# Kernel tuning notes

Hardware: AMD Instinct MI355X
Metric: run time of the kernel (lower is better)

## Reference

```python
import jax, jax.numpy as jnp
import numpy as np

N, C, T, V = 64, 64, 256, 25
REL, OUT = 8, 64
ALPHA = 1.0


def setup_inputs() -> dict:
    key = jax.random.key(0)
    ks = jax.random.split(key, 10)
    s = lambda k, shape: jax.random.normal(k, shape, dtype=jnp.float32) * 0.05
    return {
        "x": jax.random.normal(ks[0], (N, C, T, V), dtype=jnp.float32),
        "A": jax.random.normal(ks[1], (V, V), dtype=jnp.float32),
        "w1": s(ks[2], (REL, C)), "b1": s(ks[3], (REL,)),
        "w2": s(ks[4], (REL, C)), "b2": s(ks[5], (REL,)),
        "w3": s(ks[6], (OUT, C)), "b3": s(ks[7], (OUT,)),
        "w4": s(ks[8], (OUT, REL)), "b4": s(ks[9], (OUT,)),
    }


def reference(x, A, w1, b1, w2, b2, w3, b3, w4, b4):
    # 1x1 conv commutes with the temporal mean, so reduce T first (same math).
    xm = jnp.mean(x, axis=2)                                   # [N, C, V]
    x1 = jnp.einsum('ncv,rc->nrv', xm, w1) + b1[:, None]        # [N, R, V]
    x2 = jnp.einsum('ncv,rc->nrv', xm, w2) + b2[:, None]        # [N, R, V]
    x3 = jnp.einsum('nctv,oc->notv', x, w3) + b3[:, None, None] # [N, O, T, V]
    # dynamic topology: tanh of broadcast difference -> [N, R, V, V]
    adj = jnp.tanh(x1[:, :, :, None] - x2[:, :, None, :])
    # conv4 (1x1 over VxV) then scale + static adjacency
    d = jnp.einsum('nruv,or->nouv', adj, w4) + b4[:, None, None]
    d = d * ALPHA + A[None, None]                               # [N, O, V, V]
    # graph aggregation: out[n,o,t,v] = sum_u d[n,o,u,v] * x3[n,o,t,u]
    return jnp.einsum('nouv,notu->notv', d, x3)
```

## Files before the change

### kernel.cpp

```cpp
#include <hip/hip_runtime.h>

#define N_ 64
#define C_ 64
#define T_ 256
#define V_ 25
#define R_ 8
#define O_ 64
constexpr int TV = T_ * V_;
constexpr float INV_T = 1.0f / (float)T_;
constexpr int TC = 16;
constexpr int NPOS = TC * V_;
constexpr int NT = NPOS / 16;
constexpr int DP = 32;
constexpr int UPAD = 40;
constexpr int X3S = 16 * UPAD + 8;
constexpr int LS = 402;

typedef __attribute__((ext_vector_type(8))) short s8v;
typedef __attribute__((ext_vector_type(4))) float f4v;

__device__ __forceinline__ unsigned short f2bf(float f) {
    union { float f; unsigned u; } v; v.f = f;
    unsigned r = v.u + 0x7FFFu + ((v.u >> 16) & 1u);
    return (unsigned short)(r >> 16);
}
__device__ __forceinline__ unsigned pk2(float a, float b) {
    return (unsigned)f2bf(a) | ((unsigned)f2bf(b) << 16);
}
__device__ __forceinline__ float bf2f(unsigned short h) {
    union { unsigned u; float f; } v; v.u = (unsigned)h << 16; return v.f;
}

__global__ __launch_bounds__(512) void k_prep(const float* __restrict__ x,
                                              float* __restrict__ xm,
                                              float* out) {
    __shared__ unsigned short lx[C_ * LS];
    const int n   = blockIdx.y;
    const int tc  = blockIdx.x;
    const int tid = threadIdx.x;
    const float* xb = x + (size_t)n * C_ * TV + tc * NPOS;
    char* xTb = (char*)out + (size_t)n * O_ * TV * 4 + (size_t)tc * 1600;

    #pragma unroll 4
    for (int i = 0; i < 13; ++i) {
        const int s = i * 512 + tid;
        if (s < C_ * 100) {
            const int c = s / 100, p4 = s - c * 100;
            const f4v v = *(const f4v*)(xb + (size_t)c * TV + p4 * 4);
            unsigned* p = (unsigned*)&lx[c * LS + p4 * 4];
            p[0] = pk2(v[0], v[1]);
            p[1] = pk2(v[2], v[3]);
        }
    }
    __syncthreads();

    #pragma unroll
    for (int i = 0; i < 4; ++i) {
        const int p = i * 512 + tid;
        if (p < C_ * V_) {
            const int c = p / V_, v = p - c * V_;
            float s = 0.f;
            #pragma unroll
            for (int t = 0; t < TC; ++t) s += bf2f(lx[c * LS + t * V_ + v]);
            atomicAdd(&xm[(size_t)n * C_ * V_ + p], s * INV_T);
        }
    }

    #pragma unroll 2
    for (int i = 0; i < 7; ++i) {
        const int it = i * 512 + tid;
        if (it < 3200) {
            const int pos = it >> 3, ch = it & 7;
            s8v pk;
            #pragma unroll
            for (int j = 0; j < 8; ++j)
                pk[j] = (short)lx[(ch * 8 + j) * LS + pos];
            const int L = pos * 128 + ch * 16;
            const int row = L / 1600, off = L - row * 1600;
            *(s8v*)(xTb + (size_t)row * (TV * 4) + off) = pk;
        }
    }
}

__global__ __launch_bounds__(256) void k_dmat(const float* __restrict__ xm,
                                              const float* __restrict__ A,
                                              const float* __restrict__ w1,
                                              const float* __restrict__ b1,
                                              const float* __restrict__ w2,
                                              const float* __restrict__ b2,
                                              const float* __restrict__ w4,
                                              const float* __restrict__ b4,
                                              unsigned short* __restrict__ dT) {
    __shared__ float xms[C_][V_];
    __shared__ float x1s[R_][V_];
    __shared__ float x2s[R_][V_];
    const int n  = blockIdx.x;
    const int og = blockIdx.y * 8;
    const int tid = threadIdx.x;

    for (int i = tid; i < C_ * V_; i += 256)
        xms[i / V_][i % V_] = xm[(size_t)n * C_ * V_ + i];
    __syncthreads();

    for (int i = tid; i < 2 * R_ * V_; i += 256) {
        const int j = i % (R_ * V_);
        const int r = j / V_, v = j % V_;
        const bool first = (i < R_ * V_);
        const float* w = first ? w1 : w2;
        float acc = first ? b1[r] : b2[r];
        #pragma unroll
        for (int c = 0; c < C_; ++c) acc += w[r * C_ + c] * xms[c][v];
        if (first) x1s[r][v] = acc;
        else       x2s[r][v] = acc;
    }
    __syncthreads();

    unsigned short* dn = dT + (size_t)n * O_ * DP * DP;
    for (int p = tid; p < DP * DP; p += 256) {
        const int v = p >> 5, u = p & 31;
        if (u < V_ && v < V_) {
            float adjr[R_];
            #pragma unroll
            for (int r = 0; r < R_; ++r) adjr[r] = tanhf(x1s[r][u] - x2s[r][v]);
            const float a = A[u * V_ + v];
            #pragma unroll
            for (int oo = 0; oo < 8; ++oo) {
                const int o = og + oo;
                float acc = b4[o];
                #pragma unroll
                for (int r = 0; r < R_; ++r) acc = fmaf(w4[o * R_ + r], adjr[r], acc);
                dn[(size_t)o * DP * DP + p] = f2bf(acc + a);
            }
        } else {
            #pragma unroll
            for (int oo = 0; oo < 8; ++oo)
                dn[(size_t)(og + oo) * DP * DP + p] = 0;
        }
    }
}

__global__ __launch_bounds__(512) void k_F(const float* __restrict__ w3,
                                           const float* __restrict__ b3,
                                           const unsigned short* __restrict__ dT,
                                           float* io) {
    __shared__ __align__(16) unsigned short x3b[16 * X3S];

    const int n    = blockIdx.y;
    const int tc   = blockIdx.x;
    const int tid  = threadIdx.x;
    const int lane = tid & 63;
    const int wave = tid >> 6;
    const int l16  = lane & 15;
    const int lg   = lane >> 4;

    if (tid < 256) {
        const int o_l = tid >> 4, t = tid & 15;
        *(s8v*)&x3b[o_l * X3S + t * UPAD + 24] = (s8v)0;
    }
    __syncthreads();

    const char* xTb = (const char*)io + (size_t)n * O_ * TV * 4 + (size_t)tc * 1600;
    s8v bfr[4][2];
    #pragma unroll
    for (int i = 0; i < 4; ++i) {
        const int nt = wave + 8 * i;
        if (nt < NT) {
            const int pos = nt * 16 + l16;
            #pragma unroll
            for (int kh = 0; kh < 2; ++kh) {
                const int L = pos * 128 + kh * 64 + lg * 16;
                const int row = L / 1600, off = L - row * 1600;
                bfr[i][kh] = *(const s8v*)(xTb + (size_t)row * (TV * 4) + off);
            }
        }
    }

    const unsigned short* dn = dT + (size_t)n * O_ * DP * DP;
    float* on = io + (size_t)n * O_ * TV + tc * NPOS;

    #pragma unroll 1
    for (int h = 0; h < 4; ++h) {
        s8v afr[2];
        #pragma unroll
        for (int kh = 0; kh < 2; ++kh) {
            const float* wp = w3 + (h * 16 + l16) * C_ + kh * 32 + lg * 8;
            s8v f;
            #pragma unroll
            for (int j = 0; j < 8; ++j) f[j] = (short)f2bf(wp[j]);
            afr[kh] = f;
        }
        const f4v b3h = *(const f4v*)(b3 + h * 16 + lg * 4);

        #pragma unroll
        for (int i = 0; i < 4; ++i) {
            const int nt = wave + 8 * i;
            if (nt < NT) {
                const int pos = nt * 16 + l16;
                const int t = pos / 25, u = pos - 25 * t;
                f4v acc = (f4v)0.f;
                acc = __builtin_amdgcn_mfma_f32_16x16x32_bf16(afr[0], bfr[i][0], acc, 0, 0, 0);
                acc = __builtin_amdgcn_mfma_f32_16x16x32_bf16(afr[1], bfr[i][1], acc, 0, 0, 0);
                #pragma unroll
                for (int r = 0; r < 4; ++r)
                    x3b[(lg * 4 + r) * X3S + t * UPAD + u] = f2bf(acc[r] + b3h[r]);
            }
        }
        __syncthreads();

        #pragma unroll
        for (int oo = 0; oo < 2; ++oo) {
            const int o_l = wave * 2 + oo;
            const int o_g = h * 16 + o_l;
            const unsigned short* dp = dn + (size_t)o_g * DP * DP;
            const s8v bv0 = *(const s8v*)(dp + l16 * DP + lg * 8);
            const s8v bv1 = *(const s8v*)(dp + (16 + l16) * DP + lg * 8);
            const s8v av  = *(const s8v*)&x3b[o_l * X3S + l16 * UPAD + lg * 8];
            f4v c0 = (f4v)0.f, c1 = (f4v)0.f;
            c0 = __builtin_amdgcn_mfma_f32_16x16x32_bf16(av, bv0, c0, 0, 0, 0);
            c1 = __builtin_amdgcn_mfma_f32_16x16x32_bf16(av, bv1, c1, 0, 0, 0);
            float* ob = on + (size_t)o_g * TV;
            #pragma unroll
            for (int r = 0; r < 4; ++r) {
                const int t = lg * 4 + r;
                ob[t * 25 + l16] = c0[r];
                if (l16 < 9) ob[t * 25 + 16 + l16] = c1[r];
            }
        }
        __syncthreads();
    }
}

extern "C" void kernel_launch(void* const* d_in, const int* in_sizes, int n_in,
                              void* d_out, int out_size, void* d_ws, size_t ws_size,
                              hipStream_t stream) {
    const float* x  = (const float*)d_in[0];
    const float* A  = (const float*)d_in[1];
    const float* w1 = (const float*)d_in[2];
    const float* b1 = (const float*)d_in[3];
    const float* w2 = (const float*)d_in[4];
    const float* b2 = (const float*)d_in[5];
    const float* w3 = (const float*)d_in[6];
    const float* b3 = (const float*)d_in[7];
    const float* w4 = (const float*)d_in[8];
    const float* b4 = (const float*)d_in[9];

    float* out = (float*)d_out;
    float* xm  = (float*)d_ws;
    unsigned short* dTm = (unsigned short*)(xm + (size_t)N_ * C_ * V_);

    hipMemsetAsync(xm, 0, (size_t)N_ * C_ * V_ * sizeof(float), stream);
    k_prep<<<dim3(T_ / TC, N_), 512, 0, stream>>>(x, xm, out);
    k_dmat<<<dim3(N_, 8), 256, 0, stream>>>(xm, A, w1, b1, w2, b2, w4, b4, dTm);
    k_F<<<dim3(T_ / TC, N_), 512, 0, stream>>>(w3, b3, dTm, out);
}
```

Before: 97.45 us.

## Replace LDS transpose and temporal reduction in prep kernel with MFMA identity/selector matmuls

The prep kernel no longer stages x in shared memory. Each wave loads bf16-packed fragments straight into registers. It uses MFMA against an identity matrix to transpose channels into the packed output layout, and MFMA against a position-mod-25 selector matrix to accumulate the temporal sums per joint. This removes the LDS round trip, the __syncthreads barrier and the strided LDS reads. In exchange it adds redundant matrix-core work, narrower 8-byte global stores, and clamped overlapping loads on the last chunk.

```diff
diff --git a/kernel.cpp b/kernel.cpp
--- a/kernel.cpp
+++ b/kernel.cpp
@@ -14,10 +14,10 @@
 constexpr int DP = 32;
 constexpr int UPAD = 40;
 constexpr int X3S = 16 * UPAD + 8;
-constexpr int LS = 402;
 
 typedef __attribute__((ext_vector_type(8))) short s8v;
 typedef __attribute__((ext_vector_type(4))) float f4v;
+typedef __attribute__((ext_vector_type(2))) unsigned u2v;
 
 __device__ __forceinline__ unsigned short f2bf(float f) {
     union { float f; unsigned u; } v; v.f = f;
@@ -27,58 +27,92 @@
 __device__ __forceinline__ unsigned pk2(float a, float b) {
     return (unsigned)f2bf(a) | ((unsigned)f2bf(b) << 16);
 }
-__device__ __forceinline__ float bf2f(unsigned short h) {
-    union { unsigned u; float f; } v; v.u = (unsigned)h << 16; return v.f;
-}
 
 __global__ __launch_bounds__(512) void k_prep(const float* __restrict__ x,
                                               float* __restrict__ xm,
                                               float* out) {
-    __shared__ unsigned short lx[C_ * LS];
-    const int n   = blockIdx.y;
-    const int tc  = blockIdx.x;
-    const int tid = threadIdx.x;
-    const float* xb = x + (size_t)n * C_ * TV + tc * NPOS;
+    const int n    = blockIdx.y;
+    const int tc   = blockIdx.x;
+    const int tid  = threadIdx.x;
+    const int lane = tid & 63;
+    const int wave = tid >> 6;
+    const int cq   = wave & 3;
+    const int half = wave >> 2;
+    const int l16  = lane & 15;
+    const int lg   = lane >> 4;
+
+    const float* xr = x + (size_t)(n * C_ + cq * 16 + l16) * TV + tc * NPOS;
     char* xTb = (char*)out + (size_t)n * O_ * TV * 4 + (size_t)tc * 1600;
 
-    #pragma unroll 4
-    for (int i = 0; i < 13; ++i) {
-        const int s = i * 512 + tid;
-        if (s < C_ * 100) {
-            const int c = s / 100, p4 = s - c * 100;
-            const f4v v = *(const f4v*)(xb + (size_t)c * TV + p4 * 4);
-            unsigned* p = (unsigned*)&lx[c * LS + p4 * 4];
-            p[0] = pk2(v[0], v[1]);
-            p[1] = pk2(v[2], v[3]);
-        }
-    }
-    __syncthreads();
-
+    s8v bi_lo, bi_hi;
     #pragma unroll
-    for (int i = 0; i < 4; ++i) {
-        const int p = i * 512 + tid;
-        if (p < C_ * V_) {
-            const int c = p / V_, v = p - c * V_;
-            float s = 0.f;
-            #pragma unroll
-            for (int t = 0; t < TC; ++t) s += bf2f(lx[c * LS + t * V_ + v]);
-            atomicAdd(&xm[(size_t)n * C_ * V_ + p], s * INV_T);
-        }
-    }
-
-    #pragma unroll 2
-    for (int i = 0; i < 7; ++i) {
-        const int it = i * 512 + tid;
-        if (it < 3200) {
-            const int pos = it >> 3, ch = it & 7;
-            s8v pk;
-            #pragma unroll
-            for (int j = 0; j < 8; ++j)
-                pk[j] = (short)lx[(ch * 8 + j) * LS + pos];
-            const int L = pos * 128 + ch * 16;
-            const int row = L / 1600, off = L - row * 1600;
-            *(s8v*)(xTb + (size_t)row * (TV * 4) + off) = pk;
-        }
+    for (int j = 0; j < 8; ++j) {
+        const int k = lg * 8 + j;
+        bi_lo[j] = (short)((k == l16)      ? 0x3F80 : 0);
+        bi_hi[j] = (short)((k == l16 + 16) ? 0x3F80 : 0);
+    }
+
+    f4v acc0 = (f4v)0.f, acc1 = (f4v)0.f;
+
+    const int ch0 = half * 7, ch1 = half ? 13 : 7;
+    #pragma unroll 1
+    for (int ch = ch0; ch < ch1; ++ch) {
+        const int posbase = ch * 32;
+        int off = posbase + lg * 8;
+        if (off >= NPOS) off = NPOS - 16;
+        const f4v xa = *(const f4v*)(xr + off);
+        const f4v xb = *(const f4v*)(xr + off + 4);
+        s8v afr;
+        {
+            unsigned* ap = (unsigned*)&afr;
+            ap[0] = pk2(xa[0], xa[1]); ap[1] = pk2(xa[2], xa[3]);
+            ap[2] = pk2(xb[0], xb[1]); ap[3] = pk2(xb[2], xb[3]);
+        }
+
+        f4v c0 = (f4v)0.f, c1 = (f4v)0.f;
+        c0 = __builtin_amdgcn_mfma_f32_16x16x32_bf16(afr, bi_lo, c0, 0, 0, 0);
+        c1 = __builtin_amdgcn_mfma_f32_16x16x32_bf16(afr, bi_hi, c1, 0, 0, 0);
+
+        s8v bm_lo, bm_hi;
+        {
+            const int kb = posbase + lg * 8;
+            int m = kb % 25;
+            #pragma unroll
+            for (int j = 0; j < 8; ++j) {
+                const bool valid = (kb + j) < NPOS;
+                bm_lo[j] = (short)((valid && m == l16)      ? 0x3F80 : 0);
+                bm_hi[j] = (short)((valid && m == l16 + 16) ? 0x3F80 : 0);
+                if (++m == 25) m = 0;
+            }
+        }
+        acc0 = __builtin_amdgcn_mfma_f32_16x16x32_bf16(afr, bm_lo, acc0, 0, 0, 0);
+        acc1 = __builtin_amdgcn_mfma_f32_16x16x32_bf16(afr, bm_hi, acc1, 0, 0, 0);
+
+        {
+            const int pos = posbase + l16;
+            const int L = pos * 128 + (cq * 16 + lg * 4) * 2;
+            const int row = L / 1600, o = L - row * 1600;
+            *(u2v*)(xTb + (size_t)row * (TV * 4) + o) =
+                u2v{pk2(c0[0], c0[1]), pk2(c0[2], c0[3])};
+        }
+        if (posbase + 16 + l16 < NPOS) {
+            const int pos = posbase + 16 + l16;
+            const int L = pos * 128 + (cq * 16 + lg * 4) * 2;
+            const int row = L / 1600, o = L - row * 1600;
+            *(u2v*)(xTb + (size_t)row * (TV * 4) + o) =
+                u2v{pk2(c1[0], c1[1]), pk2(c1[2], c1[3])};
+        }
+    }
+
+    const int cb = cq * 16 + lg * 4;
+    float* xb0 = xm + (size_t)n * C_ * V_;
+    #pragma unroll
+    for (int r = 0; r < 4; ++r)
+        atomicAdd(&xb0[(cb + r) * V_ + l16], acc0[r] * INV_T);
+    if (l16 < 9) {
+        #pragma unroll
+        for (int r = 0; r < 4; ++r)
+            atomicAdd(&xb0[(cb + r) * V_ + 16 + l16], acc1[r] * INV_T);
     }
 }
 
```

Result: slower. 110.6 us (+13.5%).

## Split prep blocks in half and replace atomic mean with partial-sum reduction kernel

Applied to the files above, without the earlier changes.

Each prep block now handles half of a 16-timestep chunk (200 positions) with 256 threads, doubling the grid and halving shared memory per block. Instead of atomically accumulating the temporal mean into a zeroed buffer, each block writes its per-block partial sums to a workspace, and a new reduction kernel sums the 32 partials per sample. This removes the memset and the atomic contention, and may raise occupancy. The cost is an extra kernel launch and additional workspace traffic for the partial sums.

```diff
diff --git a/kernel.cpp b/kernel.cpp
--- a/kernel.cpp
+++ b/kernel.cpp
@@ -14,7 +14,8 @@
 constexpr int DP = 32;
 constexpr int UPAD = 40;
 constexpr int X3S = 16 * UPAD + 8;
-constexpr int LS = 402;
+constexpr int CV = C_ * V_;
+constexpr int LSTR = 210;
 
 typedef __attribute__((ext_vector_type(8))) short s8v;
 typedef __attribute__((ext_vector_type(4))) float f4v;
@@ -31,54 +32,73 @@
     union { unsigned u; float f; } v; v.u = (unsigned)h << 16; return v.f;
 }
 
-__global__ __launch_bounds__(512) void k_prep(const float* __restrict__ x,
-                                              float* __restrict__ xm,
+__global__ __launch_bounds__(256) void k_prep(const float* __restrict__ x,
+                                              float* __restrict__ xmp,
                                               float* out) {
-    __shared__ unsigned short lx[C_ * LS];
-    const int n   = blockIdx.y;
-    const int tc  = blockIdx.x;
-    const int tid = threadIdx.x;
-    const float* xb = x + (size_t)n * C_ * TV + tc * NPOS;
+    __shared__ unsigned short lx[C_ * LSTR];
+    const int n    = blockIdx.y;
+    const int ph   = blockIdx.x;
+    const int tid  = threadIdx.x;
+    const int tc   = ph >> 1;
+    const int poff = (ph & 1) * 200;
+
+    const float* xb = x + (size_t)n * C_ * TV + tc * NPOS + poff;
     char* xTb = (char*)out + (size_t)n * O_ * TV * 4 + (size_t)tc * 1600;
 
-    #pragma unroll 4
+    #pragma unroll
     for (int i = 0; i < 13; ++i) {
-        const int s = i * 512 + tid;
-        if (s < C_ * 100) {
-            const int c = s / 100, p4 = s - c * 100;
+        const int s = i * 256 + tid;
+        if (s < 3200) {
+            const int c = s / 50, p4 = s - c * 50;
             const f4v v = *(const f4v*)(xb + (size_t)c * TV + p4 * 4);
-            unsigned* p = (unsigned*)&lx[c * LS + p4 * 4];
+            unsigned* p = (unsigned*)&lx[c * LSTR + p4 * 4];
             p[0] = pk2(v[0], v[1]);
             p[1] = pk2(v[2], v[3]);
         }
     }
     __syncthreads();
 
-    #pragma unroll
-    for (int i = 0; i < 4; ++i) {
-        const int p = i * 512 + tid;
-        if (p < C_ * V_) {
+    #pragma unroll 2
+    for (int i = 0; i < 7; ++i) {
+        const int it = i * 256 + tid;
+        if (it < 1600) {
+            const int pos = it >> 3, cg = it & 7;
+            s8v pk;
+            #pragma unroll
+            for (int j = 0; j < 8; ++j)
+                pk[j] = (short)lx[(cg * 8 + j) * LSTR + pos];
+            const int L = (poff + pos) * 128 + cg * 16;
+            const int row = L / 1600, off = L - row * 1600;
+            *(s8v*)(xTb + (size_t)row * (TV * 4) + off) = pk;
+        }
+    }
+
+    float* xp = xmp + (size_t)(n * 32 + ph) * CV;
+    #pragma unroll 2
+    for (int i = 0; i < 7; ++i) {
+        const int p = i * 256 + tid;
+        if (p < CV) {
             const int c = p / V_, v = p - c * V_;
             float s = 0.f;
             #pragma unroll
-            for (int t = 0; t < TC; ++t) s += bf2f(lx[c * LS + t * V_ + v]);
-            atomicAdd(&xm[(size_t)n * C_ * V_ + p], s * INV_T);
-        }
-    }
-
-    #pragma unroll 2
-    for (int i = 0; i < 7; ++i) {
-        const int it = i * 512 + tid;
-        if (it < 3200) {
-            const int pos = it >> 3, ch = it & 7;
-            s8v pk;
-            #pragma unroll
-            for (int j = 0; j < 8; ++j)
-                pk[j] = (short)lx[(ch * 8 + j) * LS + pos];
-            const int L = pos * 128 + ch * 16;
-            const int row = L / 1600, off = L - row * 1600;
-            *(s8v*)(xTb + (size_t)row * (TV * 4) + off) = pk;
-        }
+            for (int t = 0; t < 8; ++t) s += bf2f(lx[c * LSTR + t * V_ + v]);
+            xp[p] = s;
+        }
+    }
+}
+
+__global__ __launch_bounds__(256) void k_red(const float* __restrict__ xmp,
+                                             float* __restrict__ xm) {
+    const int n   = blockIdx.x >> 2;
+    const int sg  = blockIdx.x & 3;
+    const int i0  = sg * 400;
+    const int tid = threadIdx.x;
+    const float* base = xmp + (size_t)n * 32 * CV;
+    for (int i = i0 + tid; i < i0 + 400; i += 256) {
+        float s = 0.f;
+        #pragma unroll
+        for (int t = 0; t < 32; ++t) s += base[t * CV + i];
+        xm[(size_t)n * CV + i] = s * INV_T;
     }
 }
 
@@ -246,10 +266,11 @@
 
     float* out = (float*)d_out;
     float* xm  = (float*)d_ws;
-    unsigned short* dTm = (unsigned short*)(xm + (size_t)N_ * C_ * V_);
-
-    hipMemsetAsync(xm, 0, (size_t)N_ * C_ * V_ * sizeof(float), stream);
-    k_prep<<<dim3(T_ / TC, N_), 512, 0, stream>>>(x, xm, out);
+    unsigned short* dTm = (unsigned short*)(xm + (size_t)N_ * CV);
+    float* xmp = (float*)(dTm + (size_t)N_ * O_ * DP * DP);
+
+    k_prep<<<dim3(32, N_), 256, 0, stream>>>(x, xmp, out);
+    k_red<<<N_ * 4, 256, 0, stream>>>(xmp, xm);
     k_dmat<<<dim3(N_, 8), 256, 0, stream>>>(xm, A, w1, b1, w2, b2, w4, b4, dTm);
     k_F<<<dim3(T_ / TC, N_), 512, 0, stream>>>(w3, b3, dTm, out);
 }
```

Result: no change. 97.43 us (-0.0%).
